# Performance work log

Hardware: AMD Instinct MI355X
Metric: run time of the kernel (lower is better)

The kernel has to match this reference:

```python
import jax, jax.numpy as jnp
import numpy as np

N_RAYS = 8192
AABB_LO, AABB_HI = -1.5, 1.5
GRID = 300
STEP_RATIO = 3.0
DIST_SCALE = 25.0
W_THRES = 1e-4
NEAR, FAR = 0.05, 6.0
NUM_SEM, DIM_INST = 20, 16
H_DEN, H_APP, F_APP, F_SEM = 64, 64, 27, 32

_EXT = AABB_HI - AABB_LO
STEP_SIZE = (_EXT / (GRID - 1 + 0.001)) * STEP_RATIO          # update_step_size
N_SAMPLES = int(np.sqrt(3.0) * _EXT / STEP_SIZE) + 1          # 173


def setup_inputs() -> dict:
    key = jax.random.key(0)
    ks = jax.random.split(key, 12)
    o = jax.random.normal(ks[0], (N_RAYS, 3), jnp.float32)
    o = 4.0 * o / jnp.linalg.norm(o, axis=-1, keepdims=True)      # camera origins on radius-4 sphere
    tgt = jax.random.uniform(ks[1], (N_RAYS, 3), jnp.float32, minval=-0.5, maxval=0.5)
    d = tgt - o
    d = d / jnp.linalg.norm(d, axis=-1, keepdims=True)            # unit viewdirs through the box
    rays = jnp.concatenate([o, d], -1)
    g = lambda k, shp, fan: jax.random.normal(k, shp, jnp.float32) / np.sqrt(fan)
    return {
        'rays': rays,
        'Wd1': g(ks[2], (3, H_DEN), 3), 'bd1': jnp.zeros((H_DEN,), jnp.float32),
        'Wd2': g(ks[3], (H_DEN, 1), H_DEN), 'bd2': jnp.zeros((1,), jnp.float32),
        'Wapp': g(ks[4], (3, F_APP), 3),
        'Wa1': g(ks[5], (F_APP + 3, H_APP), F_APP + 3), 'ba1': jnp.zeros((H_APP,), jnp.float32),
        'Wa2': g(ks[6], (H_APP, 3), H_APP), 'ba2': jnp.zeros((3,), jnp.float32),
        'Wsf': g(ks[7], (3, F_SEM), 3),
        'Wsm': g(ks[8], (F_SEM, NUM_SEM), F_SEM), 'bsm': jnp.zeros((NUM_SEM,), jnp.float32),
        'Wi': g(ks[9], (3, DIM_INST), 3),
        'perturb': 0, 'white_bg': 1, 'is_train': 0,
    }


def _render(rays, Wd1, bd1, Wd2, bd2, Wapp, Wa1, ba1, Wa2, ba2, Wsf, Wsm, bsm, Wi,
            white_bg):
    lo = jnp.full((3,), AABB_LO, rays.dtype)
    hi = jnp.full((3,), AABB_HI, rays.dtype)
    o, d = rays[:, :3], rays[:, 3:6]
    # --- sample_points_in_box (TensoRF sample_ray, perturb=0) ---
    vec = jnp.where(d == 0, 1e-6, d)
    rate_a = (hi - o) / vec
    rate_b = (lo - o) / vec
    t_min = jnp.clip(jnp.minimum(rate_a, rate_b).max(-1), NEAR, FAR)       # [N]
    rng = jnp.arange(N_SAMPLES, dtype=rays.dtype)
    z_vals = t_min[:, None] + rng[None, :] * STEP_SIZE                     # [N,S]
    xyz = o[:, None, :] + d[:, None, :] * z_vals[..., None]                # [N,S,3]
    mask_xyz = jnp.all((xyz >= lo) & (xyz <= hi), -1)                      # [N,S]
    dists = jnp.concatenate([z_vals[:, 1:] - z_vals[:, :-1],
                             jnp.zeros_like(z_vals[:, :1])], -1)
    mid = jnp.concatenate([(z_vals[:, 1:] + z_vals[:, :-1]) * 0.5,
                           z_vals[:, -2:-1]], -1)
    # --- normalize_coordinates ---
    xyzn = (xyz - lo) * (2.0 / _EXT) - 1.0
    # --- density (masked query -> dense compute + where, same values) ---
    h = jax.nn.relu(xyzn @ Wd1 + bd1)                                      # [N,S,Hd]
    sigma = jnp.where(mask_xyz, jax.nn.softplus((h @ Wd2 + bd2)[..., 0]), 0.0)
    # --- raw_to_alpha ---
    alpha = 1.0 - jnp.exp(-sigma * (dists * DIST_SCALE))                   # [N,S]
    T = jnp.cumprod(jnp.concatenate([jnp.ones_like(alpha[:, :1]),
                                     1.0 - alpha + 1e-10], -1), -1)
    weight = alpha * T[:, :-1]
    # --- eff_distloss(weight, mid, dists) ---
    loss_uni = (dists * weight * weight).sum(-1).mean() / 3.0
    wm = weight * mid
    w_cs = jnp.cumsum(weight, -1)
    wm_cs = jnp.cumsum(wm, -1)
    loss_bi = 2.0 * (wm[:, 1:] * w_cs[:, :-1] - weight[:, 1:] * wm_cs[:, :-1]).sum(-1).mean()
    dist_reg = loss_uni + loss_bi
    # --- appearance / semantics / instances on appearance_mask ---
    app_mask = weight > W_THRES
    viewdirs = jnp.broadcast_to(d[:, None, :], xyz.shape)
    feat = xyzn @ Wapp                                                     # [N,S,27]
    ha = jax.nn.relu(jnp.concatenate([feat, viewdirs], -1) @ Wa1 + ba1)    # [N,S,Ha]
    rgb = jnp.where(app_mask[..., None], jax.nn.sigmoid(ha @ Wa2 + ba2), 0.0)
    sem = jnp.where(app_mask[..., None], (xyzn @ Wsf) @ Wsm + bsm, 0.0)
    inst = jnp.where(app_mask[..., None], xyzn @ Wi, 0.0)
    # --- compositing ---
    opacity = weight.sum(-1)
    rgb_map = (weight[..., None] * rgb).sum(-2)
    depth_map = (weight * z_vals).sum(-1)
    w = jax.lax.stop_gradient(weight)[..., None]                           # stop_semantic_grad
    semantics = (w * sem).sum(-2)
    instances = (w * inst).sum(-2)                                          # is_train=False
    if white_bg:
        rgb_map = rgb_map + (1.0 - opacity[..., None])
    rgb_map = jnp.clip(rgb_map, 0.0, 1.0)
    return rgb_map, semantics, instances, depth_map, dist_reg


def reference(rays, Wd1, bd1, Wd2, bd2, Wapp, Wa1, ba1, Wa2, ba2, Wsf, Wsm, bsm, Wi,
              perturb, white_bg, is_train):
    return _render(rays, Wd1, bd1, Wd2, bd2, Wapp, Wa1, ba1, Wa2, ba2,
                   Wsf, Wsm, bsm, Wi, bool(white_bg))
```

## Files before the change

kernel.cpp:

```cpp
#include <hip/hip_runtime.h>

#define NRAYS 8192
#define NSAMP 173
#define LASTI 172
#define NBLK  (NRAYS / 4)

__device__ __forceinline__ float RL(float x, int u) {
    return __int_as_float(__builtin_amdgcn_readlane(__float_as_int(x), u));
}

template <int CTRL, int RM, bool BC>
__device__ __forceinline__ float updpp(float old, float x) {
    return __int_as_float(__builtin_amdgcn_update_dpp(
        __float_as_int(old), __float_as_int(x), CTRL, RM, 0xf, BC));
}

__device__ __forceinline__ float scan_add64(float x) {
    x += updpp<0x111, 0xf, true>(0.f, x);
    x += updpp<0x112, 0xf, true>(0.f, x);
    x += updpp<0x114, 0xf, true>(0.f, x);
    x += updpp<0x118, 0xf, true>(0.f, x);
    x += updpp<0x142, 0xa, true>(0.f, x);
    x += updpp<0x143, 0xc, true>(0.f, x);
    return x;
}

__device__ __forceinline__ float scan_mul64(float x) {
    x *= updpp<0x111, 0xf, false>(1.f, x);
    x *= updpp<0x112, 0xf, false>(1.f, x);
    x *= updpp<0x114, 0xf, false>(1.f, x);
    x *= updpp<0x118, 0xf, false>(1.f, x);
    x *= updpp<0x142, 0xa, false>(1.f, x);
    x *= updpp<0x143, 0xc, false>(1.f, x);
    return x;
}

__device__ __forceinline__ float wave_sum64(float v) {
    return RL(scan_add64(v), 63);
}

__device__ __forceinline__ float softplus_f(float x) {
    if (x > 15.f) return x;
    return __logf(1.f + __expf(x));
}
__device__ __forceinline__ float sigmoid_f(float x) {
    return 1.f / (1.f + __expf(-x));
}

__global__ void prep_kernel(
    const float* __restrict__ Wd1, const float* __restrict__ bd1,
    const float* __restrict__ Wd2, const float* __restrict__ bd2,
    const float* __restrict__ Wapp, const float* __restrict__ Wa1,
    const float* __restrict__ ba1, const float* __restrict__ Wa2,
    const float* __restrict__ ba2, const float* __restrict__ Wsf,
    const float* __restrict__ Wsm, const float* __restrict__ bsm,
    const float* __restrict__ Wi, float* __restrict__ prep)
{
    const int t = threadIdx.x;
    if (t < 64) {
        ((float4*)prep)[t] = make_float4(Wd1[t], Wd1[64 + t], Wd1[128 + t], bd1[t]);
        prep[256 + t] = Wd2[t];
        ((float4*)(prep + 320))[t] =
            make_float4(Wa1[27 * 64 + t], Wa1[28 * 64 + t], Wa1[29 * 64 + t], ba1[t]);
    } else if (t < 128) {
        int u = t - 64;
        prep[832 + 2 * u]     = Wa2[3 * u + 1];
        prep[832 + 2 * u + 1] = Wa2[3 * u + 2];
    } else if (t < 192) {
        int u = t - 128;
        float s0 = 0.f, s1 = 0.f, s2 = 0.f;
        for (int j = 0; j < 27; ++j) {
            float w = Wa1[j * 64 + u];
            s0 = fmaf(Wapp[j], w, s0);
            s1 = fmaf(Wapp[27 + j], w, s1);
            s2 = fmaf(Wapp[54 + j], w, s2);
        }
        ((float4*)(prep + 576))[u] = make_float4(s0, s1, s2, Wa2[3 * u]);
    } else {
        for (int job = t - 192; job < 132; job += 64) {
            if (job < 60) {
                int m = job / 20, s = job % 20;
                float a = 0.f;
                for (int k = 0; k < 32; ++k) a = fmaf(Wsf[m * 32 + k], Wsm[k * 20 + s], a);
                prep[960 + job] = a;
            } else if (job < 80) {
                prep[1020 + (job - 60)] = bsm[job - 60];
            } else if (job < 128) {
                prep[1040 + (job - 80)] = Wi[job - 80];
            } else if (job == 128) {
                prep[1088] = bd2[0];
            } else {
                prep[1089 + (job - 129)] = ba2[job - 129];
            }
        }
    }
}

__launch_bounds__(256, 4)
__global__ void render_kernel(
    const float* __restrict__ rays,
    const float* __restrict__ prep,
    const int* __restrict__ whitebg_p,
    float* __restrict__ out,
    float* __restrict__ wsdist)
{
    __shared__ float4 qd4[64];
    __shared__ float  wd2s[64];

    const int t = threadIdx.x;
    const int wid = t >> 6, lane = t & 63;
    const int r = blockIdx.x * 4 + wid;

    if (t < 64) {
        qd4[t] = ((const float4*)prep)[t];
        wd2s[t] = prep[256 + t];
    }

    const float4* __restrict__ apAg = (const float4*)(prep + 576);
    const float2* __restrict__ apBg = (const float2*)(prep + 832);

    const float o0 = rays[r * 6 + 0], o1 = rays[r * 6 + 1], o2 = rays[r * 6 + 2];
    const float d0 = rays[r * 6 + 3], d1 = rays[r * 6 + 4], d2 = rays[r * 6 + 5];

    float tm;
    {
        float v0 = (d0 == 0.f) ? 1e-6f : d0;
        float v1 = (d1 == 0.f) ? 1e-6f : d1;
        float v2 = (d2 == 0.f) ? 1e-6f : d2;
        float a0 = __fdiv_rn(__fsub_rn(1.5f, o0), v0), b0 = __fdiv_rn(__fsub_rn(-1.5f, o0), v0);
        float a1 = __fdiv_rn(__fsub_rn(1.5f, o1), v1), b1 = __fdiv_rn(__fsub_rn(-1.5f, o1), v1);
        float a2 = __fdiv_rn(__fsub_rn(1.5f, o2), v2), b2 = __fdiv_rn(__fsub_rn(-1.5f, o2), v2);
        float m0 = fminf(a0, b0), m1 = fminf(a1, b1), m2 = fminf(a2, b2);
        tm = fmaxf(fmaxf(m0, m1), m2);
        tm = fminf(fmaxf(tm, 0.05f), 6.0f);
    }

    float dcr;
    {
        float4 dp = ((const float4*)(prep + 320))[lane];
        dcr = fmaf(d2, dp.z, fmaf(d1, dp.y, fmaf(d0, dp.x, dp.w)));
    }
    __syncthreads();

    const float bd2c = prep[1088];
    const float ba2c0 = prep[1089], ba2c1 = prep[1090], ba2c2 = prep[1091];

    const float STEPF = (float)(3.0 / 299.001 * 3.0);
    const float zlast2 = __fadd_rn(tm, __fmul_rn(171.f, STEPF));

    float aR0 = 0.f, aR1 = 0.f, aR2 = 0.f;
    float aS0 = 0.f, aS1 = 0.f, aS2 = 0.f;
    float aSw = 0.f;
    float aD = 0.f, aLu = 0.f, aLb = 0.f;
    float Tc = 1.f, Wcar = 0.f, WMc = 0.f;

    {
        const int iA = lane, iB = 64 + lane;
        float zA = __fadd_rn(tm, __fmul_rn((float)iA, STEPF));
        float zB = __fadd_rn(tm, __fmul_rn((float)iB, STEPF));
        float xA0 = __fadd_rn(o0, __fmul_rn(d0, zA));
        float xA1 = __fadd_rn(o1, __fmul_rn(d1, zA));
        float xA2 = __fadd_rn(o2, __fmul_rn(d2, zA));
        float xB0 = __fadd_rn(o0, __fmul_rn(d0, zB));
        float xB1 = __fadd_rn(o1, __fmul_rn(d1, zB));
        float xB2 = __fadd_rn(o2, __fmul_rn(d2, zB));
        bool inA = (xA0 >= -1.5f) && (xA0 <= 1.5f) && (xA1 >= -1.5f) && (xA1 <= 1.5f) &&
                   (xA2 >= -1.5f) && (xA2 <= 1.5f);
        bool inB = (xB0 >= -1.5f) && (xB0 <= 1.5f) && (xB1 >= -1.5f) && (xB1 <= 1.5f) &&
                   (xB2 >= -1.5f) && (xB2 <= 1.5f);

        float xnA0 = xA0 * (2.f / 3.f), xnA1 = xA1 * (2.f / 3.f), xnA2 = xA2 * (2.f / 3.f);
        float xnB0 = xB0 * (2.f / 3.f), xnB1 = xB1 * (2.f / 3.f), xnB2 = xB2 * (2.f / 3.f);

        float spA = bd2c, spB = bd2c;
#pragma unroll 8
        for (int u = 0; u < 64; ++u) {
            float4 q = qd4[u];
            float w2 = wd2s[u];
            float hA = fmaf(xnA0, q.x, fmaf(xnA1, q.y, fmaf(xnA2, q.z, q.w)));
            float hB = fmaf(xnB0, q.x, fmaf(xnB1, q.y, fmaf(xnB2, q.z, q.w)));
            spA = fmaf(fmaxf(hA, 0.f), w2, spA);
            spB = fmaf(fmaxf(hB, 0.f), w2, spB);
        }
        float sigA = inA ? softplus_f(spA) : 0.f;
        float sigB = inB ? softplus_f(spB) : 0.f;

        float zAn = __fadd_rn(tm, __fmul_rn((float)(iA + 1), STEPF));
        float zBn = __fadd_rn(tm, __fmul_rn((float)(iB + 1), STEPF));
        float distA = __fsub_rn(zAn, zA);
        float distB = __fsub_rn(zBn, zB);
        float alA = 1.f - __expf(-sigA * distA * 25.f);
        float alB = 1.f - __expf(-sigB * distB * 25.f);
        float fA = 1.f - alA + 1e-10f;
        float fB = 1.f - alB + 1e-10f;

        float pA = scan_mul64(fA);
        float pB = scan_mul64(fB);
        float pexA = updpp<0x138, 0xf, false>(1.f, pA);
        float pexB = updpp<0x138, 0xf, false>(1.f, pB);
        float TA = Tc * pexA;
        float wA = alA * TA;
        float TcB = Tc * RL(pA, 63);
        float TB = TcB * pexB;
        float wB = alB * TB;

        float midA = 0.5f * __fadd_rn(zA, zAn);
        float midB = 0.5f * __fadd_rn(zB, zBn);
        float wmA = wA * midA;
        float wmB = wB * midB;

        float swA = scan_add64(wA), smA = scan_add64(wmA);
        float swB = scan_add64(wB), smB = scan_add64(wmB);
        float wexA = updpp<0x138, 0xf, true>(0.f, swA);
        float wmexA = updpp<0x138, 0xf, true>(0.f, smA);
        float wexB = updpp<0x138, 0xf, true>(0.f, swB);
        float wmexB = updpp<0x138, 0xf, true>(0.f, smB);

        aLb += wmA * (Wcar + wexA) - wA * (WMc + wmexA);
        aLu = fmaf(distA * wA, wA, aLu);
        aD = fmaf(wA, zA, aD);
        float WcarB = Wcar + RL(swA, 63);
        float WMcB = WMc + RL(smA, 63);
        aLb += wmB * (WcarB + wexB) - wB * (WMcB + wmexB);
        aLu = fmaf(distB * wB, wB, aLu);
        aD = fmaf(wB, zB, aD);

        Tc = TcB * RL(pB, 63);
        Wcar = WcarB + RL(swB, 63);
        WMc = WMcB + RL(smB, 63);

        float wapA = (wA > 1e-4f) ? wA : 0.f;
        float wapB = (wB > 1e-4f) ? wB : 0.f;
        if (__ballot(wapA > 0.f) != 0ull) {
            float c0 = 0.f, c1 = 0.f, c2 = 0.f;
#pragma unroll 8
            for (int u = 0; u < 64; ++u) {
                float4 A4 = apAg[u];
                float2 B2 = apBg[u];
                float dcu = RL(dcr, u);
                float h = fmaf(xnA0, A4.x, fmaf(xnA1, A4.y, fmaf(xnA2, A4.z, dcu)));
                h = fmaxf(h, 0.f);
                c0 = fmaf(h, A4.w, c0);
                c1 = fmaf(h, B2.x, c1);
                c2 = fmaf(h, B2.y, c2);
            }
            aR0 = fmaf(wapA, sigmoid_f(c0 + ba2c0), aR0);
            aR1 = fmaf(wapA, sigmoid_f(c1 + ba2c1), aR1);
            aR2 = fmaf(wapA, sigmoid_f(c2 + ba2c2), aR2);
            aS0 = fmaf(wapA, xnA0, aS0);
            aS1 = fmaf(wapA, xnA1, aS1);
            aS2 = fmaf(wapA, xnA2, aS2);
            aSw += wapA;
        }
        if (__ballot(wapB > 0.f) != 0ull) {
            float c0 = 0.f, c1 = 0.f, c2 = 0.f;
#pragma unroll 8
            for (int u = 0; u < 64; ++u) {
                float4 A4 = apAg[u];
                float2 B2 = apBg[u];
                float dcu = RL(dcr, u);
                float h = fmaf(xnB0, A4.x, fmaf(xnB1, A4.y, fmaf(xnB2, A4.z, dcu)));
                h = fmaxf(h, 0.f);
                c0 = fmaf(h, A4.w, c0);
                c1 = fmaf(h, B2.x, c1);
                c2 = fmaf(h, B2.y, c2);
            }
            aR0 = fmaf(wapB, sigmoid_f(c0 + ba2c0), aR0);
            aR1 = fmaf(wapB, sigmoid_f(c1 + ba2c1), aR1);
            aR2 = fmaf(wapB, sigmoid_f(c2 + ba2c2), aR2);
            aS0 = fmaf(wapB, xnB0, aS0);
            aS1 = fmaf(wapB, xnB1, aS1);
            aS2 = fmaf(wapB, xnB2, aS2);
            aSw += wapB;
        }
    }

    if (Tc >= 1e-8f) {
        int i = 128 + lane;
        bool valid = i < NSAMP;
        float z = __fadd_rn(tm, __fmul_rn((float)i, STEPF));
        float x0 = __fadd_rn(o0, __fmul_rn(d0, z));
        float x1 = __fadd_rn(o1, __fmul_rn(d1, z));
        float x2 = __fadd_rn(o2, __fmul_rn(d2, z));
        bool inbox = valid && (x0 >= -1.5f) && (x0 <= 1.5f) && (x1 >= -1.5f) && (x1 <= 1.5f) &&
                     (x2 >= -1.5f) && (x2 <= 1.5f);
        if (__ballot(inbox) != 0ull) {
            float xn0 = x0 * (2.f / 3.f), xn1 = x1 * (2.f / 3.f), xn2 = x2 * (2.f / 3.f);

            float sp = bd2c;
#pragma unroll 8
            for (int u = 0; u < 64; ++u) {
                float4 q = qd4[u];
                float h = fmaf(xn0, q.x, fmaf(xn1, q.y, fmaf(xn2, q.z, q.w)));
                sp = fmaf(fmaxf(h, 0.f), wd2s[u], sp);
            }
            float sigma = inbox ? softplus_f(sp) : 0.f;

            float znext = __fadd_rn(tm, __fmul_rn((float)(i + 1), STEPF));
            float dist = (i < LASTI) ? __fsub_rn(znext, z) : 0.f;
            float alpha = 1.f - __expf(-sigma * dist * 25.f);
            float f = 1.f - alpha + 1e-10f;

            float p = scan_mul64(f);
            float pex = updpp<0x138, 0xf, false>(1.f, p);
            float T = Tc * pex;
            float w = alpha * T;

            float mid = (i < LASTI) ? 0.5f * __fadd_rn(z, znext) : zlast2;
            float wm = w * mid;

            float sw = scan_add64(w);
            float swm = scan_add64(wm);
            float wex = updpp<0x138, 0xf, true>(0.f, sw);
            float wmex = updpp<0x138, 0xf, true>(0.f, swm);

            aLb += wm * (Wcar + wex) - w * (WMc + wmex);
            aLu = fmaf(dist * w, w, aLu);
            aD = fmaf(w, z, aD);
            Wcar += RL(sw, 63);
            WMc += RL(swm, 63);

            float wapp = (w > 1e-4f) ? w : 0.f;
            if (__ballot(wapp > 0.f) != 0ull) {
                float c0 = 0.f, c1 = 0.f, c2 = 0.f;
#pragma unroll 8
                for (int u = 0; u < 64; ++u) {
                    float4 A4 = apAg[u];
                    float2 B2 = apBg[u];
                    float dcu = RL(dcr, u);
                    float h = fmaf(xn0, A4.x, fmaf(xn1, A4.y, fmaf(xn2, A4.z, dcu)));
                    h = fmaxf(h, 0.f);
                    c0 = fmaf(h, A4.w, c0);
                    c1 = fmaf(h, B2.x, c1);
                    c2 = fmaf(h, B2.y, c2);
                }
                aR0 = fmaf(wapp, sigmoid_f(c0 + ba2c0), aR0);
                aR1 = fmaf(wapp, sigmoid_f(c1 + ba2c1), aR1);
                aR2 = fmaf(wapp, sigmoid_f(c2 + ba2c2), aR2);
                aS0 = fmaf(wapp, xn0, aS0);
                aS1 = fmaf(wapp, xn1, aS1);
                aS2 = fmaf(wapp, xn2, aS2);
                aSw += wapp;
            }
        }
    }

    aR0 = wave_sum64(aR0); aR1 = wave_sum64(aR1); aR2 = wave_sum64(aR2);
    aS0 = wave_sum64(aS0); aS1 = wave_sum64(aS1); aS2 = wave_sum64(aS2);
    aSw = wave_sum64(aSw);
    aD = wave_sum64(aD);
    aLu = wave_sum64(aLu);
    aLb = wave_sum64(aLb);

    float opac = Wcar;
    int wb = *whitebg_p;
    float bg = wb ? (1.f - opac) : 0.f;

    float* out_rgb = out;
    float* out_sem = out + 24576;
    float* out_inst = out + 188416;
    float* out_dep = out + 319488;

    if (lane < 3) {
        float rv = (lane == 0 ? aR0 : (lane == 1 ? aR1 : aR2)) + bg;
        rv = fminf(fmaxf(rv, 0.f), 1.f);
        out_rgb[r * 3 + lane] = rv;
    }
    if (lane < 20) {
        float sv = aS0 * prep[960 + lane] + aS1 * prep[980 + lane] + aS2 * prep[1000 + lane] +
                   aSw * prep[1020 + lane];
        out_sem[r * 20 + lane] = sv;
    }
    if (lane < 16) {
        float iv = aS0 * prep[1040 + lane] + aS1 * prep[1056 + lane] + aS2 * prep[1072 + lane];
        out_inst[r * 16 + lane] = iv;
    }
    if (lane == 0) {
        out_dep[r] = aD;
        wsdist[r] = aLu * (1.f / 3.f) + 2.f * aLb;
    }
}

__global__ void reduce_dist_kernel(const float* __restrict__ ws, float* __restrict__ out) {
    __shared__ float sm[256];
    int t = threadIdx.x;
    float a = 0.f;
    const float4* w4 = (const float4*)ws;
    for (int i = t; i < NRAYS / 4; i += 256) {
        float4 v = w4[i];
        a += (v.x + v.y) + (v.z + v.w);
    }
    sm[t] = a;
    __syncthreads();
    for (int st = 128; st > 0; st >>= 1) {
        if (t < st) sm[t] += sm[t + st];
        __syncthreads();
    }
    if (t == 0) out[0] = sm[0] * (1.f / (float)NRAYS);
}

extern "C" void kernel_launch(void* const* d_in, const int* in_sizes, int n_in,
                              void* d_out, int out_size, void* d_ws, size_t ws_size,
                              hipStream_t stream) {
    const float* rays = (const float*)d_in[0];
    const float* Wd1  = (const float*)d_in[1];
    const float* bd1  = (const float*)d_in[2];
    const float* Wd2  = (const float*)d_in[3];
    const float* bd2  = (const float*)d_in[4];
    const float* Wapp = (const float*)d_in[5];
    const float* Wa1  = (const float*)d_in[6];
    const float* ba1  = (const float*)d_in[7];
    const float* Wa2  = (const float*)d_in[8];
    const float* ba2  = (const float*)d_in[9];
    const float* Wsf  = (const float*)d_in[10];
    const float* Wsm  = (const float*)d_in[11];
    const float* bsm  = (const float*)d_in[12];
    const float* Wi   = (const float*)d_in[13];
    const int* wb     = (const int*)d_in[15];

    float* out = (float*)d_out;
    float* prep = (float*)d_ws;
    float* wsd  = prep + 2048;

    prep_kernel<<<1, 256, 0, stream>>>(Wd1, bd1, Wd2, bd2, Wapp, Wa1, ba1, Wa2, ba2,
                                       Wsf, Wsm, bsm, Wi, prep);
    render_kernel<<<NBLK, 256, 0, stream>>>(rays, prep, wb, out, wsd);
    reduce_dist_kernel<<<1, 256, 0, stream>>>(wsd, out + 327680);
}
```

Baseline: 34.45 us.

## Fuse weight-prep kernel into render kernel and stage MLP weights in LDS

Removes the separate single-block prep kernel and has every render block compute the folded weight tables itself, storing them in shared memory. The appearance MLP inner loop now reads weights from LDS instead of global memory. This drops one kernel launch and the serialization between the prep and render kernels. In exchange, each of the 2048 blocks repeats the prep work, including a 27-term and a 32-term dot product per thread, which lengthens each block's prologue.

```diff
diff --git a/kernel.cpp b/kernel.cpp
--- a/kernel.cpp
+++ b/kernel.cpp
@@ -47,25 +47,37 @@
     return 1.f / (1.f + __expf(-x));
 }
 
-__global__ void prep_kernel(
+__launch_bounds__(256, 4)
+__global__ void render_kernel(
+    const float* __restrict__ rays,
     const float* __restrict__ Wd1, const float* __restrict__ bd1,
     const float* __restrict__ Wd2, const float* __restrict__ bd2,
     const float* __restrict__ Wapp, const float* __restrict__ Wa1,
     const float* __restrict__ ba1, const float* __restrict__ Wa2,
     const float* __restrict__ ba2, const float* __restrict__ Wsf,
     const float* __restrict__ Wsm, const float* __restrict__ bsm,
-    const float* __restrict__ Wi, float* __restrict__ prep)
+    const float* __restrict__ Wi,
+    const int* __restrict__ whitebg_p,
+    float* __restrict__ out,
+    float* __restrict__ wsdist)
 {
+    __shared__ float4 qd4[64];
+    __shared__ float  wd2s[64];
+    __shared__ float4 apAs[64];
+    __shared__ float2 apBs[64];
+    __shared__ float  wscs[60];
+    __shared__ float  bsmS[20];
+
     const int t = threadIdx.x;
+    const int wid = t >> 6, lane = t & 63;
+    const int r = blockIdx.x * 4 + wid;
+
     if (t < 64) {
-        ((float4*)prep)[t] = make_float4(Wd1[t], Wd1[64 + t], Wd1[128 + t], bd1[t]);
-        prep[256 + t] = Wd2[t];
-        ((float4*)(prep + 320))[t] =
-            make_float4(Wa1[27 * 64 + t], Wa1[28 * 64 + t], Wa1[29 * 64 + t], ba1[t]);
+        qd4[t] = make_float4(Wd1[t], Wd1[64 + t], Wd1[128 + t], bd1[t]);
+        wd2s[t] = Wd2[t];
     } else if (t < 128) {
         int u = t - 64;
-        prep[832 + 2 * u]     = Wa2[3 * u + 1];
-        prep[832 + 2 * u + 1] = Wa2[3 * u + 2];
+        apBs[u] = make_float2(Wa2[3 * u + 1], Wa2[3 * u + 2]);
     } else if (t < 192) {
         int u = t - 128;
         float s0 = 0.f, s1 = 0.f, s2 = 0.f;
@@ -75,49 +87,19 @@
             s1 = fmaf(Wapp[27 + j], w, s1);
             s2 = fmaf(Wapp[54 + j], w, s2);
         }
-        ((float4*)(prep + 576))[u] = make_float4(s0, s1, s2, Wa2[3 * u]);
+        apAs[u] = make_float4(s0, s1, s2, Wa2[3 * u]);
     } else {
-        for (int job = t - 192; job < 132; job += 64) {
+        for (int job = t - 192; job < 80; job += 64) {
             if (job < 60) {
                 int m = job / 20, s = job % 20;
                 float a = 0.f;
                 for (int k = 0; k < 32; ++k) a = fmaf(Wsf[m * 32 + k], Wsm[k * 20 + s], a);
-                prep[960 + job] = a;
-            } else if (job < 80) {
-                prep[1020 + (job - 60)] = bsm[job - 60];
-            } else if (job < 128) {
-                prep[1040 + (job - 80)] = Wi[job - 80];
-            } else if (job == 128) {
-                prep[1088] = bd2[0];
+                wscs[job] = a;
             } else {
-                prep[1089 + (job - 129)] = ba2[job - 129];
+                bsmS[job - 60] = bsm[job - 60];
             }
         }
     }
-}
-
-__launch_bounds__(256, 4)
-__global__ void render_kernel(
-    const float* __restrict__ rays,
-    const float* __restrict__ prep,
-    const int* __restrict__ whitebg_p,
-    float* __restrict__ out,
-    float* __restrict__ wsdist)
-{
-    __shared__ float4 qd4[64];
-    __shared__ float  wd2s[64];
-
-    const int t = threadIdx.x;
-    const int wid = t >> 6, lane = t & 63;
-    const int r = blockIdx.x * 4 + wid;
-
-    if (t < 64) {
-        qd4[t] = ((const float4*)prep)[t];
-        wd2s[t] = prep[256 + t];
-    }
-
-    const float4* __restrict__ apAg = (const float4*)(prep + 576);
-    const float2* __restrict__ apBg = (const float2*)(prep + 832);
 
     const float o0 = rays[r * 6 + 0], o1 = rays[r * 6 + 1], o2 = rays[r * 6 + 2];
     const float d0 = rays[r * 6 + 3], d1 = rays[r * 6 + 4], d2 = rays[r * 6 + 5];
@@ -137,13 +119,17 @@
 
     float dcr;
     {
-        float4 dp = ((const float4*)(prep + 320))[lane];
-        dcr = fmaf(d2, dp.z, fmaf(d1, dp.y, fmaf(d0, dp.x, dp.w)));
-    }
+        float b = ba1[lane];
+        b = fmaf(d0, Wa1[27 * 64 + lane], b);
+        b = fmaf(d1, Wa1[28 * 64 + lane], b);
+        b = fmaf(d2, Wa1[29 * 64 + lane], b);
+        dcr = b;
+    }
+
+    const float bd2c = bd2[0];
+    const float ba2c0 = ba2[0], ba2c1 = ba2[1], ba2c2 = ba2[2];
+
     __syncthreads();
-
-    const float bd2c = prep[1088];
-    const float ba2c0 = prep[1089], ba2c1 = prep[1090], ba2c2 = prep[1091];
 
     const float STEPF = (float)(3.0 / 299.001 * 3.0);
     const float zlast2 = __fadd_rn(tm, __fmul_rn(171.f, STEPF));
@@ -235,8 +221,8 @@
             float c0 = 0.f, c1 = 0.f, c2 = 0.f;
 #pragma unroll 8
             for (int u = 0; u < 64; ++u) {
-                float4 A4 = apAg[u];
-                float2 B2 = apBg[u];
+                float4 A4 = apAs[u];
+                float2 B2 = apBs[u];
                 float dcu = RL(dcr, u);
                 float h = fmaf(xnA0, A4.x, fmaf(xnA1, A4.y, fmaf(xnA2, A4.z, dcu)));
                 h = fmaxf(h, 0.f);
@@ -256,8 +242,8 @@
             float c0 = 0.f, c1 = 0.f, c2 = 0.f;
 #pragma unroll 8
             for (int u = 0; u < 64; ++u) {
-                float4 A4 = apAg[u];
-                float2 B2 = apBg[u];
+                float4 A4 = apAs[u];
+                float2 B2 = apBs[u];
                 float dcu = RL(dcr, u);
                 float h = fmaf(xnB0, A4.x, fmaf(xnB1, A4.y, fmaf(xnB2, A4.z, dcu)));
                 h = fmaxf(h, 0.f);
@@ -325,8 +311,8 @@
                 float c0 = 0.f, c1 = 0.f, c2 = 0.f;
 #pragma unroll 8
                 for (int u = 0; u < 64; ++u) {
-                    float4 A4 = apAg[u];
-                    float2 B2 = apBg[u];
+                    float4 A4 = apAs[u];
+                    float2 B2 = apBs[u];
                     float dcu = RL(dcr, u);
                     float h = fmaf(xn0, A4.x, fmaf(xn1, A4.y, fmaf(xn2, A4.z, dcu)));
                     h = fmaxf(h, 0.f);
@@ -367,12 +353,12 @@
         out_rgb[r * 3 + lane] = rv;
     }
     if (lane < 20) {
-        float sv = aS0 * prep[960 + lane] + aS1 * prep[980 + lane] + aS2 * prep[1000 + lane] +
-                   aSw * prep[1020 + lane];
+        float sv = aS0 * wscs[lane] + aS1 * wscs[20 + lane] + aS2 * wscs[40 + lane] +
+                   aSw * bsmS[lane];
         out_sem[r * 20 + lane] = sv;
     }
     if (lane < 16) {
-        float iv = aS0 * prep[1040 + lane] + aS1 * prep[1056 + lane] + aS2 * prep[1072 + lane];
+        float iv = aS0 * Wi[lane] + aS1 * Wi[16 + lane] + aS2 * Wi[32 + lane];
         out_inst[r * 16 + lane] = iv;
     }
     if (lane == 0) {
@@ -419,11 +405,9 @@
     const int* wb     = (const int*)d_in[15];
 
     float* out = (float*)d_out;
-    float* prep = (float*)d_ws;
-    float* wsd  = prep + 2048;
-
-    prep_kernel<<<1, 256, 0, stream>>>(Wd1, bd1, Wd2, bd2, Wapp, Wa1, ba1, Wa2, ba2,
-                                       Wsf, Wsm, bsm, Wi, prep);
-    render_kernel<<<NBLK, 256, 0, stream>>>(rays, prep, wb, out, wsd);
+    float* wsd = (float*)d_ws;
+
+    render_kernel<<<NBLK, 256, 0, stream>>>(rays, Wd1, bd1, Wd2, bd2, Wapp, Wa1, ba1,
+                                            Wa2, ba2, Wsf, Wsm, bsm, Wi, wb, out, wsd);
     reduce_dist_kernel<<<1, 256, 0, stream>>>(wsd, out + 327680);
 }
```

New measurement: 31.83 us. 7.6% less time.
